# Optimization experiments

Hardware: AMD Instinct MI355X
Metric: run time of the kernel (lower is better)

## Reference

```python
import jax, jax.numpy as jnp
import numpy as np

DS = 32          # decoder_size
DIM = 512        # decoder_dim
NH = 8           # num_heads
HD = DIM // NH   # head_size = 64
NE = 4           # num_enc_reshape
NC = 2           # num_classes
B = 8
L = 2            # transformer layers
FF = 4 * DIM


def _ln(x, g, b):
    m = x.mean(-1, keepdims=True)
    v = x.var(-1, keepdims=True)
    return (x - m) / jnp.sqrt(v + 1e-5) * g + b


def _pos_bias(x_emb, y_emb, pad0, pad1):
    # 2D relative position encoding gathered from embeddings, shape [S2,S2,HD]
    ix = jnp.tile(jnp.arange(DS), DS)                       # column index per pixel
    iy = jnp.repeat(jnp.arange(DS), DS)                     # row index per pixel
    xd = jnp.clip(ix[None, :] - ix[:, None], -DS, DS) + DS  # [S2,S2] in [1,2*DS-1]
    yd = jnp.clip(iy[None, :] - iy[:, None], -DS, DS) + DS
    pos = x_emb[xd] + y_emb[yd]                              # [S2,S2,HD]
    S2 = DS * DS
    p0 = jnp.broadcast_to(pad0, (NE, NE, HD))
    p1 = jnp.broadcast_to(pad1, (S2, NE, HD))
    pos_pad = jnp.concatenate([p0, p1], axis=0)              # [S,NE,HD]
    right = jnp.concatenate([jnp.transpose(p1, (1, 0, 2)), pos], axis=0)  # [S,S2,HD]
    return jnp.concatenate([pos_pad, right], axis=1)         # [S,S,HD]


def _forward(x, patches, We, be, x_emb, y_emb, pad0, pad1,
             Wq, bq, Wk, bk, Wv, bv, Wo, bo,
             ln1_g, ln1_b, ln2_g, ln2_b, W1, b1, W2, b2, Wc, bc):
    b = x.shape[0]
    # patch embedding: [B,3,H,W] -> [B,H,W,3] -> Linear(3,DIM) -> [B,S2,DIM]
    p = jnp.transpose(patches, (0, 2, 3, 1))
    px = (p @ We + be).reshape(b, -1, DIM)
    xe = x.reshape(b, NE, DIM)
    h = jnp.concatenate([xe, px], axis=1)                    # [B,S,DIM]
    pos = _pos_bias(x_emb, y_emb, pad0, pad1)                # [S,S,HD]
    scale = 1.0 / jnp.sqrt(jnp.float32(HD))
    for l in range(L):
        hn = _ln(h, ln1_g[l], ln1_b[l])
        q = (hn @ Wq[l] + bq[l]).reshape(b, -1, NH, HD) * scale
        k = (hn @ Wk[l] + bk[l]).reshape(b, -1, NH, HD)
        v = (hn @ Wv[l] + bv[l]).reshape(b, -1, NH, HD)
        # content scores + gathered relative-position structure bias
        scores = jnp.einsum('bihd,bjhd->bhij', q, k) + jnp.einsum('bihd,ijd->bhij', q, pos)
        attn = jax.nn.softmax(scores, axis=-1)
        o = jnp.einsum('bhij,bjhd->bihd', attn, v).reshape(b, -1, DIM)
        h = h + (o @ Wo[l] + bo[l])
        hn = _ln(h, ln2_g[l], ln2_b[l])
        h = h + (jax.nn.relu(hn @ W1[l] + b1[l]) @ W2[l] + b2[l])
    out = h[:, NE:, :] @ Wc + bc                             # [B,S2,NC]
    out = out.reshape(b, DS, DS, NC)
    return jnp.transpose(out, (0, 3, 1, 2))                  # [B,NC,DS,DS]


def setup_inputs() -> dict:
    key = jax.random.key(0)
    ks = jax.random.split(key, 24)
    s = 0.02
    d = {}
    d['x'] = jax.random.normal(ks[0], (B, NE * DIM), jnp.float32)
    d['patches'] = jax.random.normal(ks[1], (B, 3, DS, DS), jnp.float32)
    d['We'] = jax.random.normal(ks[2], (3, DIM), jnp.float32) * s
    d['be'] = jnp.zeros((DIM,), jnp.float32)
    d['x_emb'] = jax.random.normal(ks[3], (2 * DS, HD), jnp.float32) * s
    d['y_emb'] = jax.random.normal(ks[4], (2 * DS, HD), jnp.float32) * s
    d['pad0'] = jax.random.normal(ks[5], (1, 1, HD), jnp.float32) * s
    d['pad1'] = jax.random.normal(ks[6], (1, 1, HD), jnp.float32) * s
    d['Wq'] = jax.random.normal(ks[7], (L, DIM, DIM), jnp.float32) * s
    d['bq'] = jnp.zeros((L, DIM), jnp.float32)
    d['Wk'] = jax.random.normal(ks[8], (L, DIM, DIM), jnp.float32) * s
    d['bk'] = jnp.zeros((L, DIM), jnp.float32)
    d['Wv'] = jax.random.normal(ks[9], (L, DIM, DIM), jnp.float32) * s
    d['bv'] = jnp.zeros((L, DIM), jnp.float32)
    d['Wo'] = jax.random.normal(ks[10], (L, DIM, DIM), jnp.float32) * s
    d['bo'] = jnp.zeros((L, DIM), jnp.float32)
    d['ln1_g'] = jnp.ones((L, DIM), jnp.float32)
    d['ln1_b'] = jnp.zeros((L, DIM), jnp.float32)
    d['ln2_g'] = jnp.ones((L, DIM), jnp.float32)
    d['ln2_b'] = jnp.zeros((L, DIM), jnp.float32)
    d['W1'] = jax.random.normal(ks[11], (L, DIM, FF), jnp.float32) * s
    d['b1'] = jnp.zeros((L, FF), jnp.float32)
    d['W2'] = jax.random.normal(ks[12], (L, FF, DIM), jnp.float32) * s
    d['b2'] = jnp.zeros((L, DIM), jnp.float32)
    d['Wc'] = jax.random.normal(ks[13], (DIM, NC), jnp.float32) * s
    d['bc'] = jnp.zeros((NC,), jnp.float32)
    return d


def reference(x, patches, We, be, x_emb, y_emb, pad0, pad1,
              Wq, bq, Wk, bk, Wv, bv, Wo, bo,
              ln1_g, ln1_b, ln2_g, ln2_b, W1, b1, W2, b2, Wc, bc):
    return _forward(x, patches, We, be, x_emb, y_emb, pad0, pad1,
                    Wq, bq, Wk, bk, Wv, bv, Wo, bo,
                    ln1_g, ln1_b, ln2_g, ln2_b, W1, b1, W2, b2, Wc, bc)
```

## Files before the change

kernel.cpp:

```cpp
#include <hip/hip_runtime.h>
#include <hip/hip_bf16.h>

#define DS 32
#define DIM 512
#define NH 8
#define HD 64
#define NE 4
#define NC 2
#define BB 8
#define LL 2
#define FFD 2048
#define S2 1024
#define SS 1028
#define MM (BB*SS)
#define KE 160
#define EXT ((size_t)BB*NH*SS*KE)

typedef __attribute__((ext_vector_type(8))) short s16x8;
typedef __attribute__((ext_vector_type(4))) float f32x4;
typedef unsigned short u16;

__device__ __forceinline__ u16 f2b(float f) {
    __hip_bfloat16 h = __float2bfloat16(f);
    return *reinterpret_cast<u16*>(&h);
}
__device__ __forceinline__ float b2f(u16 u) {
    __hip_bfloat16 h;
    *reinterpret_cast<u16*>(&h) = u;
    return __bfloat162float(h);
}

__global__ void embed_kernel(const float* __restrict__ x, const float* __restrict__ patches,
                             const float* __restrict__ We, const float* __restrict__ be,
                             float* __restrict__ h) {
    int row = blockIdx.x;
    int b = row / SS, i = row % SS;
    float* hr = h + (size_t)row * DIM;
    if (i < NE) {
        const float* xr = x + (size_t)b*NE*DIM + (size_t)i*DIM;
        for (int d = threadIdx.x; d < DIM; d += blockDim.x) hr[d] = xr[d];
    } else {
        int p = i - NE;
        float c0 = patches[(size_t)b*3*S2 + 0*S2 + p];
        float c1 = patches[(size_t)b*3*S2 + 1*S2 + p];
        float c2 = patches[(size_t)b*3*S2 + 2*S2 + p];
        for (int d = threadIdx.x; d < DIM; d += blockDim.x)
            hr[d] = be[d] + c0*We[d] + c1*We[DIM+d] + c2*We[2*DIM+d];
    }
}

__global__ void ln_kernel(const float* __restrict__ in, u16* __restrict__ out,
                          const float* __restrict__ g, const float* __restrict__ bt) {
    int row = blockIdx.x;
    const float* xr = in + (size_t)row*DIM;
    int t = threadIdx.x;
    float v0 = xr[t], v1 = xr[t+256];
    float s = v0 + v1, s2 = v0*v0 + v1*v1;
    for (int off = 32; off; off >>= 1) { s += __shfl_down(s, off); s2 += __shfl_down(s2, off); }
    __shared__ float ps[4], ps2[4];
    int wid = t >> 6, lane = t & 63;
    if (lane == 0) { ps[wid] = s; ps2[wid] = s2; }
    __syncthreads();
    if (t == 0) { ps[0] = ps[0]+ps[1]+ps[2]+ps[3]; ps2[0] = ps2[0]+ps2[1]+ps2[2]+ps2[3]; }
    __syncthreads();
    float mean = ps[0] * (1.0f/DIM);
    float var  = ps2[0] * (1.0f/DIM) - mean*mean;
    float inv = rsqrtf(var + 1e-5f);
    u16* orow = out + (size_t)row*DIM;
    orow[t]     = f2b((v0 - mean)*inv*g[t]     + bt[t]);
    orow[t+256] = f2b((v1 - mean)*inv*g[t+256] + bt[t+256]);
}

__global__ void transp_kernel(const float* __restrict__ src, u16* __restrict__ dst,
                              int R, int C) {
    __shared__ float tile[32][33];
    int c0 = blockIdx.x*32, r0 = blockIdx.y*32;
    int tx = threadIdx.x & 31, ty = threadIdx.x >> 5;
    #pragma unroll
    for (int ii = 0; ii < 4; ii++)
        tile[ty + ii*8][tx] = src[(size_t)(r0 + ty + ii*8)*C + c0 + tx];
    __syncthreads();
    #pragma unroll
    for (int ii = 0; ii < 4; ii++)
        dst[(size_t)(c0 + ty + ii*8)*R + r0 + tx] = f2b(tile[tx][ty + ii*8]);
}

__global__ void cat_bias_kernel(const float* __restrict__ bq, const float* __restrict__ bk,
                                const float* __restrict__ bv, float* __restrict__ out) {
    int t = blockIdx.x*256 + threadIdx.x;
    if (t >= 1536) return;
    out[t] = (t < 512) ? bq[t] : (t < 1024 ? bk[t-512] : bv[t-1024]);
}

template<int MODE, int RELU>
__global__ __launch_bounds__(256) void mfma_gemm(
    const u16* __restrict__ A, const u16* __restrict__ WT,
    const float* __restrict__ bias, const float* __restrict__ res,
    float* __restrict__ Cf, u16* __restrict__ Cb,
    u16* __restrict__ kd, u16* __restrict__ vd,
    int M, int N, int K)
{
    __shared__ __align__(16) u16 a_lds[128*64];
    __shared__ __align__(16) u16 b_lds[128*64];
    int row0 = blockIdx.x*128, col0 = blockIdx.y*128;
    int tid = threadIdx.x, w = tid>>6, l = tid&63;
    int lg = l>>4, lc = l&15;
    int wr = (w>>1)*64, wc = (w&1)*64;
    f32x4 acc[4][4];
    #pragma unroll
    for (int m = 0; m < 4; m++)
        #pragma unroll
        for (int n = 0; n < 4; n++) { f32x4 z = {0.f,0.f,0.f,0.f}; acc[m][n] = z; }

    s16x8 ar[4], br[4];
    #pragma unroll
    for (int p = 0; p < 4; p++) {
        int e = p*256 + tid;
        int r = e >> 3, c16 = e & 7;
        int ra = row0 + r; if (ra > M-1) ra = M-1;
        ar[p] = *(const s16x8*)(A  + (size_t)ra*K + c16*8);
        br[p] = *(const s16x8*)(WT + (size_t)(col0 + r)*K + c16*8);
    }

    for (int k0 = 0; k0 < K; k0 += 64) {
        #pragma unroll
        for (int p = 0; p < 4; p++) {
            int e = p*256 + tid;
            int r = e >> 3, c16 = e & 7;
            int ldso = r*128 + ((c16*16) ^ ((r&7)<<4));
            *(s16x8*)((char*)a_lds + ldso) = ar[p];
            *(s16x8*)((char*)b_lds + ldso) = br[p];
        }
        __syncthreads();
        int kn = k0 + 64;
        if (kn < K) {
            #pragma unroll
            for (int p = 0; p < 4; p++) {
                int e = p*256 + tid;
                int r = e >> 3, c16 = e & 7;
                int ra = row0 + r; if (ra > M-1) ra = M-1;
                ar[p] = *(const s16x8*)(A  + (size_t)ra*K + kn + c16*8);
                br[p] = *(const s16x8*)(WT + (size_t)(col0 + r)*K + kn + c16*8);
            }
        }
        #pragma unroll
        for (int ks = 0; ks < 2; ks++) {
            int cb = (ks*64 + lg*16) ^ ((l&7)<<4);
            s16x8 af[4], bfr[4];
            #pragma unroll
            for (int m = 0; m < 4; m++)
                af[m] = *(const s16x8*)((const char*)a_lds + (wr + m*16 + lc)*128 + cb);
            #pragma unroll
            for (int n = 0; n < 4; n++)
                bfr[n] = *(const s16x8*)((const char*)b_lds + (wc + n*16 + lc)*128 + cb);
            #pragma unroll
            for (int m = 0; m < 4; m++)
                #pragma unroll
                for (int n = 0; n < 4; n++)
                    acc[m][n] = __builtin_amdgcn_mfma_f32_16x16x32_bf16(af[m], bfr[n], acc[m][n], 0, 0, 0);
        }
        __syncthreads();
    }
    #pragma unroll
    for (int m = 0; m < 4; m++) {
        #pragma unroll
        for (int r = 0; r < 4; r++) {
            int row = row0 + wr + m*16 + lg*4 + r;
            if (row >= M) continue;
            #pragma unroll
            for (int n = 0; n < 4; n++) {
                int col = col0 + wc + n*16 + lc;
                float v = acc[m][n][r] + bias[col];
                if (MODE == 2) {
                    int which = col >> 9, c2 = col & 511;
                    if (which == 0) v *= 0.125f;
                    u16* dst = (which == 0) ? Cb : (which == 1 ? kd : vd);
                    dst[(size_t)row*512 + c2] = f2b(v);
                } else if (MODE == 1) {
                    if (RELU) v = fmaxf(v, 0.f);
                    Cb[(size_t)row*N + col] = f2b(v);
                } else {
                    Cf[(size_t)row*N + col] = v + res[(size_t)row*N + col];
                }
            }
        }
    }
}

__global__ void qp_kernel(const u16* __restrict__ q, const float* __restrict__ pad0,
                          const float* __restrict__ pad1, float* __restrict__ qp0,
                          float* __restrict__ qp1) {
    int idx = blockIdx.x * blockDim.x + threadIdx.x;
    if (idx >= BB*NH*SS) return;
    int i = idx % SS; int bh = idx / SS; int b = bh >> 3, hh = bh & 7;
    const u16* qr = q + ((size_t)(b*SS + i))*DIM + hh*HD;
    float a0 = 0.f, a1 = 0.f;
    #pragma unroll 8
    for (int d = 0; d < HD; d++) { float qv = b2f(qr[d]); a0 += qv*pad0[d]; a1 += qv*pad1[d]; }
    qp0[idx] = a0; qp1[idx] = a1;
}

__global__ void qext_kernel(const u16* __restrict__ qb, const float* __restrict__ qp0,
                            const float* __restrict__ qp1, u16* __restrict__ Qe) {
    size_t id = (size_t)blockIdx.x*256 + threadIdx.x;
    if (id >= EXT/8) return;
    int u = (int)(id % 20);
    size_t row = id / 20;
    int bh = (int)(row / SS), i = (int)(row - (size_t)bh*SS);
    int b = bh >> 3, hh = bh & 7;
    s16x8 val = {0,0,0,0,0,0,0,0};
    if (u < 8) {
        val = *(const s16x8*)(qb + ((size_t)(b*SS + i))*DIM + hh*HD + u*8);
    } else if (u == 16) {
        float v128 = (i < NE) ? qp0[bh*SS + i] : qp1[bh*SS + i];
        float v129 = (i < NE) ? qp1[bh*SS + i] : 0.f;
        val[0] = (short)f2b(v128);
        val[1] = (short)f2b(v129);
    }
    *(s16x8*)(Qe + row*KE + u*8) = val;
}

__global__ void kext_kernel(const u16* __restrict__ kb, u16* __restrict__ Ke) {
    size_t id = (size_t)blockIdx.x*256 + threadIdx.x;
    if (id >= EXT/8) return;
    int u = (int)(id % 20);
    size_t row = id / 20;
    int bh = (int)(row / SS), j = (int)(row - (size_t)bh*SS);
    int b = bh >> 3, hh = bh & 7;
    const short ONE = 0x3F80;
    s16x8 val = {0,0,0,0,0,0,0,0};
    if (u < 8) {
        val = *(const s16x8*)(kb + ((size_t)(b*SS + j))*DIM + hh*HD + u*8);
    } else {
        int pj = j - NE, cj = pj & 31, rj = pj >> 5;
        #pragma unroll
        for (int e = 0; e < 8; e++) {
            int t = u*8 + e;
            short v = 0;
            if (j >= NE) {
                if (t < 96)       { if (cj == t-64) v = ONE; }
                else if (t < 128) { if (rj == t-96) v = ONE; }
                else if (t == 129) v = ONE;
            } else if (t == 128) v = ONE;
            val[e] = v;
        }
    }
    *(s16x8*)(Ke + row*KE + u*8) = val;
}

__global__ __launch_bounds__(256) void qxy_mfma(
    const u16* __restrict__ q, const float* __restrict__ x_emb,
    const float* __restrict__ y_emb, u16* __restrict__ Qe)
{
    int tile = blockIdx.x, bh = blockIdx.y;
    int b = bh >> 3, hh = bh & 7;
    int tid = threadIdx.x, w = tid>>6, l = tid&63;
    int lg = l>>4, lc = l&15;
    int wr = (w>>1)*64, wc = (w&1)*64;
    int pi0 = tile*128;

    f32x4 acc[4][4];
    #pragma unroll
    for (int m = 0; m < 4; m++)
        #pragma unroll
        for (int n = 0; n < 4; n++) { f32x4 z = {0.f,0.f,0.f,0.f}; acc[m][n] = z; }

    s16x8 af[4][2];
    #pragma unroll
    for (int m = 0; m < 4; m++) {
        int pi = pi0 + wr + m*16 + lc;
        const u16* qp = q + ((size_t)(b*SS + NE + pi))*DIM + hh*HD + lg*8;
        af[m][0] = *(const s16x8*)qp;
        af[m][1] = *(const s16x8*)(qp + 32);
    }
    s16x8 bf[4][2];
    #pragma unroll
    for (int n = 0; n < 4; n++) {
        int tau = wc + n*16 + lc;
        const float* ep = (tau < 64) ? (x_emb + (size_t)tau*HD) : (y_emb + (size_t)(tau-64)*HD);
        #pragma unroll
        for (int ks = 0; ks < 2; ks++) {
            const float* e8 = ep + ks*32 + lg*8;
            s16x8 bv;
            #pragma unroll
            for (int t2 = 0; t2 < 8; t2++) bv[t2] = (short)f2b(e8[t2]);
            bf[n][ks] = bv;
        }
    }
    #pragma unroll
    for (int ks = 0; ks < 2; ks++)
        #pragma unroll
        for (int m = 0; m < 4; m++)
            #pragma unroll
            for (int n = 0; n < 4; n++)
                acc[m][n] = __builtin_amdgcn_mfma_f32_16x16x32_bf16(af[m][ks], bf[n][ks], acc[m][n], 0, 0, 0);

    #pragma unroll
    for (int m = 0; m < 4; m++) {
        #pragma unroll
        for (int r = 0; r < 4; r++) {
            int pi = pi0 + wr + m*16 + lg*4 + r;
            int ci = pi & 31, ri = pi >> 5;
            size_t rowbase = ((size_t)bh*SS + NE + pi)*KE;
            #pragma unroll
            for (int n = 0; n < 4; n++) {
                int tau = wc + n*16 + lc;
                float v = acc[m][n][r];
                if (tau < 64) {
                    int c = tau + ci - 32;
                    if (c >= 0 && c < 32) Qe[rowbase + 64 + c] = f2b(v);
                } else {
                    int c = (tau - 64) + ri - 32;
                    if (c >= 0 && c < 32) Qe[rowbase + 96 + c] = f2b(v);
                }
            }
        }
    }
}

#define KT 64
#define NKT 17
#define NQT 17
__global__ __launch_bounds__(256) void attn_mfma(
    const u16* __restrict__ Qe, const u16* __restrict__ Ke,
    const u16* __restrict__ v, u16* __restrict__ o)
{
    __shared__ __align__(16) u16 Kl[64*192];
    __shared__ __align__(16) u16 Vt[64][72];
    __shared__ __align__(16) u16 Pl[4][16][72];
    int qt = blockIdx.x, bh = blockIdx.y;
    int b = bh >> 3, hh = bh & 7;
    int tid = threadIdx.x, w = tid>>6, l = tid&63;
    int lg = l>>4, lc = l&15;
    int i0w = qt*64 + w*16;
    const s16x8 zs = {0,0,0,0,0,0,0,0};

    s16x8 qa[5];
    {
        int qrow = i0w + lc; if (qrow > SS-1) qrow = SS-1;
        const u16* qp = Qe + ((size_t)bh*SS + qrow)*KE + lg*8;
        #pragma unroll
        for (int ks = 0; ks < 5; ks++) qa[ks] = *(const s16x8*)(qp + ks*32);
    }

    float m_[4] = {-1e30f, -1e30f, -1e30f, -1e30f};
    float l_[4] = {0.f, 0.f, 0.f, 0.f};
    f32x4 oacc[4];
    #pragma unroll
    for (int f = 0; f < 4; f++) { f32x4 z = {0.f,0.f,0.f,0.f}; oacc[f] = z; }

    int skey = tid & 63, sd0 = (tid >> 6) * 16;

    for (int kt2 = 0; kt2 < NKT; kt2++) {
        int j0 = kt2 * KT;
        #pragma unroll
        for (int p = 0; p < 5; p++) {
            int e = p*256 + tid;
            int row = e / 20, u = e - row*20;
            int j = j0 + row;
            s16x8 kv = zs;
            if (j < SS) kv = *(const s16x8*)(Ke + ((size_t)bh*SS + j)*KE + u*8);
            *(s16x8*)((char*)Kl + row*384 + ((u ^ (row&7)) << 4)) = kv;
        }
        {
            int key = j0 + skey;
            uint4 v0 = {0,0,0,0}, v1 = {0,0,0,0};
            if (key < SS) {
                const uint4* vp = (const uint4*)(v + ((size_t)(b*SS + key))*DIM + hh*HD + sd0);
                v0 = vp[0]; v1 = vp[1];
            }
            const u16* pv = (const u16*)&v0;
            #pragma unroll
            for (int jj = 0; jj < 8; jj++) Vt[sd0 + jj][skey] = pv[jj];
            pv = (const u16*)&v1;
            #pragma unroll
            for (int jj = 0; jj < 8; jj++) Vt[sd0 + 8 + jj][skey] = pv[jj];
        }
        __syncthreads();

        f32x4 s[4];
        #pragma unroll
        for (int f = 0; f < 4; f++) { f32x4 z = {0.f,0.f,0.f,0.f}; s[f] = z; }
        #pragma unroll
        for (int ks = 0; ks < 5; ks++)
            #pragma unroll
            for (int f = 0; f < 4; f++) {
                int row = f*16 + lc;
                s16x8 kb2 = *(const s16x8*)((const char*)Kl + row*384 + ((((ks<<2)+lg) ^ (row&7)) << 4));
                s[f] = __builtin_amdgcn_mfma_f32_16x16x32_bf16(qa[ks], kb2, s[f], 0, 0, 0);
            }

        #pragma unroll
        for (int r = 0; r < 4; r++) {
            #pragma unroll
            for (int f = 0; f < 4; f++) {
                int j = j0 + f*16 + lc;
                if (j >= SS) s[f][r] = -1e30f;
            }
            float t4 = fmaxf(fmaxf(s[0][r], s[1][r]), fmaxf(s[2][r], s[3][r]));
            t4 = fmaxf(t4, __shfl_xor(t4, 1));
            t4 = fmaxf(t4, __shfl_xor(t4, 2));
            t4 = fmaxf(t4, __shfl_xor(t4, 4));
            t4 = fmaxf(t4, __shfl_xor(t4, 8));
            float mn = fmaxf(m_[r], t4);
            float sc = __expf(m_[r] - mn);
            m_[r] = mn;
            float rs = 0.f;
            #pragma unroll
            for (int f = 0; f < 4; f++) {
                float p = __expf(s[f][r] - mn);
                s[f][r] = p;
                rs += p;
            }
            rs += __shfl_xor(rs, 1); rs += __shfl_xor(rs, 2);
            rs += __shfl_xor(rs, 4); rs += __shfl_xor(rs, 8);
            l_[r] = l_[r]*sc + rs;
            #pragma unroll
            for (int f = 0; f < 4; f++) oacc[f][r] *= sc;
        }
        #pragma unroll
        for (int r = 0; r < 4; r++)
            #pragma unroll
            for (int f = 0; f < 4; f++)
                Pl[w][lg*4 + r][f*16 + lc] = f2b(s[f][r]);
        #pragma unroll
        for (int ks = 0; ks < 2; ks++) {
            s16x8 pa = *(const s16x8*)&Pl[w][lc][ks*32 + lg*8];
            #pragma unroll
            for (int f = 0; f < 4; f++) {
                s16x8 vb = *(const s16x8*)&Vt[f*16 + lc][ks*32 + lg*8];
                oacc[f] = __builtin_amdgcn_mfma_f32_16x16x32_bf16(pa, vb, oacc[f], 0, 0, 0);
            }
        }
        __syncthreads();
    }
    #pragma unroll
    for (int r = 0; r < 4; r++) {
        int i = i0w + lg*4 + r;
        if (i >= SS) continue;
        float inv = 1.0f / l_[r];
        #pragma unroll
        for (int f = 0; f < 4; f++)
            o[((size_t)(b*SS + i))*DIM + hh*HD + f*16 + lc] = f2b(oacc[f][r] * inv);
    }
}

__global__ void cls_kernel(const float* __restrict__ h, const float* __restrict__ Wc,
                           const float* __restrict__ bc, float* __restrict__ out) {
    int g = blockIdx.x*4 + (threadIdx.x >> 6);
    int lane = threadIdx.x & 63;
    if (g >= BB*S2) return;
    int b = g >> 10, p = g & 1023;
    const float* hr = h + ((size_t)(b*SS + NE + p))*DIM;
    float a0 = 0.f, a1 = 0.f;
    for (int d = lane; d < DIM; d += 64) {
        float hv = hr[d];
        a0 += hv * Wc[d*NC + 0];
        a1 += hv * Wc[d*NC + 1];
    }
    for (int off = 32; off; off >>= 1) { a0 += __shfl_down(a0, off); a1 += __shfl_down(a1, off); }
    if (lane == 0) {
        out[((size_t)(b*NC + 0))*S2 + p] = a0 + bc[0];
        out[((size_t)(b*NC + 1))*S2 + p] = a1 + bc[1];
    }
}

extern "C" void kernel_launch(void* const* d_in, const int* in_sizes, int n_in,
                              void* d_out, int out_size, void* d_ws, size_t ws_size,
                              hipStream_t stream) {
    const float* x      = (const float*)d_in[0];
    const float* patches= (const float*)d_in[1];
    const float* We     = (const float*)d_in[2];
    const float* be     = (const float*)d_in[3];
    const float* x_emb  = (const float*)d_in[4];
    const float* y_emb  = (const float*)d_in[5];
    const float* pad0   = (const float*)d_in[6];
    const float* pad1   = (const float*)d_in[7];
    const float* Wq     = (const float*)d_in[8];
    const float* bq     = (const float*)d_in[9];
    const float* Wk     = (const float*)d_in[10];
    const float* bk     = (const float*)d_in[11];
    const float* Wv     = (const float*)d_in[12];
    const float* bv     = (const float*)d_in[13];
    const float* Wo     = (const float*)d_in[14];
    const float* bo     = (const float*)d_in[15];
    const float* ln1_g  = (const float*)d_in[16];
    const float* ln1_b  = (const float*)d_in[17];
    const float* ln2_g  = (const float*)d_in[18];
    const float* ln2_b  = (const float*)d_in[19];
    const float* W1     = (const float*)d_in[20];
    const float* b1     = (const float*)d_in[21];
    const float* W2     = (const float*)d_in[22];
    const float* b2     = (const float*)d_in[23];
    const float* Wc     = (const float*)d_in[24];
    const float* bc     = (const float*)d_in[25];
    float* out = (float*)d_out;

    float* ws = (float*)d_ws;
    const size_t MD = (size_t)MM*DIM;
    float* h  = ws;
    u16* hn   = (u16*)(ws + MD);
    u16* qb   = (u16*)(ws + MD + MD/2);
    u16* kb   = qb + MD;
    u16* vb   = qb + 2*MD;
    u16* ob   = qb + 3*MD;
    u16* tb   = qb;
    u16* Qe   = (u16*)(ws + 3*MD + MD/2);
    u16* Ke   = Qe + EXT;
    float* after = ws + 3*MD + MD/2 + EXT;
    float* qp0 = after;
    float* qp1 = qp0 + 65792;
    float* bqkv = qp1 + 65792;
    u16* wt   = (u16*)(bqkv + 1536);

    const size_t WL = 3145728;

    for (int l = 0; l < LL; l++) {
        u16* base = wt + (size_t)l*WL;
        transp_kernel<<<dim3(16,16), 256, 0, stream>>>(Wq + (size_t)l*DIM*DIM, base + 0,        DIM, DIM);
        transp_kernel<<<dim3(16,16), 256, 0, stream>>>(Wk + (size_t)l*DIM*DIM, base + 262144,   DIM, DIM);
        transp_kernel<<<dim3(16,16), 256, 0, stream>>>(Wv + (size_t)l*DIM*DIM, base + 524288,   DIM, DIM);
        transp_kernel<<<dim3(16,16), 256, 0, stream>>>(Wo + (size_t)l*DIM*DIM, base + 786432,   DIM, DIM);
        transp_kernel<<<dim3(64,16), 256, 0, stream>>>(W1 + (size_t)l*DIM*FFD, base + 1048576,  DIM, FFD);
        transp_kernel<<<dim3(16,64), 256, 0, stream>>>(W2 + (size_t)l*FFD*DIM, base + 2097152,  FFD, DIM);
    }

    embed_kernel<<<MM, 256, 0, stream>>>(x, patches, We, be, h);

    dim3 gQKV(65, 12);
    dim3 g512(65, 4);
    dim3 gFF (65, 16);
    const int extUnits = (int)(EXT / 8);
    const int extBlocks = (extUnits + 255) / 256;

    for (int l = 0; l < LL; l++) {
        u16* base = wt + (size_t)l*WL;
        cat_bias_kernel<<<6, 256, 0, stream>>>(bq + (size_t)l*DIM, bk + (size_t)l*DIM, bv + (size_t)l*DIM, bqkv);
        ln_kernel<<<MM, 256, 0, stream>>>(h, hn, ln1_g + l*DIM, ln1_b + l*DIM);
        mfma_gemm<2,0><<<gQKV, 256, 0, stream>>>(hn, base, bqkv, nullptr, nullptr, qb, kb, vb, MM, 1536, DIM);
        qp_kernel<<<(BB*NH*SS + 255)/256, 256, 0, stream>>>(qb, pad0, pad1, qp0, qp1);
        qext_kernel<<<extBlocks, 256, 0, stream>>>(qb, qp0, qp1, Qe);
        qxy_mfma<<<dim3(8, BB*NH), 256, 0, stream>>>(qb, x_emb, y_emb, Qe);
        kext_kernel<<<extBlocks, 256, 0, stream>>>(kb, Ke);
        attn_mfma<<<dim3(NQT, BB*NH), 256, 0, stream>>>(Qe, Ke, vb, ob);
        mfma_gemm<0,0><<<g512, 256, 0, stream>>>(ob, base + 786432, bo + (size_t)l*DIM, h, h, nullptr, nullptr, nullptr, MM, DIM, DIM);
        ln_kernel<<<MM, 256, 0, stream>>>(h, hn, ln2_g + l*DIM, ln2_b + l*DIM);
        mfma_gemm<1,1><<<gFF, 256, 0, stream>>>(hn, base + 1048576, b1 + (size_t)l*FFD, nullptr, nullptr, tb, nullptr, nullptr, MM, FFD, DIM);
        mfma_gemm<0,0><<<g512, 256, 0, stream>>>(tb, base + 2097152, b2 + (size_t)l*DIM, h, h, nullptr, nullptr, nullptr, MM, DIM, FFD);
    }

    cls_kernel<<<(BB*S2)/4, 256, 0, stream>>>(h, Wc, bc, out);
}
```

Before: 724.6 us.

## Use direct global-to-LDS loads in GEMM, XCD-aware block remap, wider attention key tiles

The GEMM now loads A/B tiles straight into LDS with global_load_lds, dropping the register staging, the software prefetch and the XOR swizzle. It also switches to a 1D grid remapped so that consecutive tiles land on the same XCD, for better L2 locality. The attention kernel processes 128 keys per iteration instead of 64, halving the loop trips and barriers, and gets a similar XCD-grouped block mapping. The risks are more LDS bank conflicts from the unswizzled layout, lost global/compute overlap in the GEMM, and higher LDS and register use in attention.

Measured after the change: 860.2 us. +18.7%, slower.

```diff
diff --git a/kernel.cpp b/kernel.cpp
--- a/kernel.cpp
+++ b/kernel.cpp
@@ -28,6 +28,13 @@
     __hip_bfloat16 h;
     *reinterpret_cast<u16*>(&h) = u;
     return __bfloat162float(h);
+}
+
+__device__ __forceinline__ void gload_lds16(const void* g, void* l) {
+    __builtin_amdgcn_global_load_lds(
+        (const __attribute__((address_space(1))) void*)(uintptr_t)g,
+        (__attribute__((address_space(3))) void*)(uint32_t)(uintptr_t)l,
+        16, 0, 0);
 }
 
 __global__ void embed_kernel(const float* __restrict__ x, const float* __restrict__ patches,
@@ -98,11 +105,17 @@
     const float* __restrict__ bias, const float* __restrict__ res,
     float* __restrict__ Cf, u16* __restrict__ Cb,
     u16* __restrict__ kd, u16* __restrict__ vd,
-    int M, int N, int K)
+    int M, int N, int K, int Nt)
 {
     __shared__ __align__(16) u16 a_lds[128*64];
     __shared__ __align__(16) u16 b_lds[128*64];
-    int row0 = blockIdx.x*128, col0 = blockIdx.y*128;
+    int nwg = gridDim.x;
+    int q8 = nwg >> 3, r8 = nwg & 7;
+    int bid = blockIdx.x;
+    int xcd = bid & 7, loc = bid >> 3;
+    int g = (xcd < r8 ? xcd*(q8+1) : r8*(q8+1) + (xcd - r8)*q8) + loc;
+    int row0 = (g / Nt) * 128, col0 = (g % Nt) * 128;
+
     int tid = threadIdx.x, w = tid>>6, l = tid&63;
     int lg = l>>4, lc = l&15;
     int wr = (w>>1)*64, wc = (w&1)*64;
@@ -112,47 +125,27 @@
         #pragma unroll
         for (int n = 0; n < 4; n++) { f32x4 z = {0.f,0.f,0.f,0.f}; acc[m][n] = z; }
 
-    s16x8 ar[4], br[4];
-    #pragma unroll
-    for (int p = 0; p < 4; p++) {
-        int e = p*256 + tid;
-        int r = e >> 3, c16 = e & 7;
-        int ra = row0 + r; if (ra > M-1) ra = M-1;
-        ar[p] = *(const s16x8*)(A  + (size_t)ra*K + c16*8);
-        br[p] = *(const s16x8*)(WT + (size_t)(col0 + r)*K + c16*8);
-    }
-
+    int c16 = l & 7;
     for (int k0 = 0; k0 < K; k0 += 64) {
         #pragma unroll
         for (int p = 0; p < 4; p++) {
             int e = p*256 + tid;
-            int r = e >> 3, c16 = e & 7;
-            int ldso = r*128 + ((c16*16) ^ ((r&7)<<4));
-            *(s16x8*)((char*)a_lds + ldso) = ar[p];
-            *(s16x8*)((char*)b_lds + ldso) = br[p];
+            int r = e >> 3;
+            int ra = row0 + r; if (ra > M-1) ra = M-1;
+            gload_lds16(A  + (size_t)ra*K + k0 + c16*8,          a_lds + p*2048 + w*512);
+            gload_lds16(WT + (size_t)(col0 + r)*K + k0 + c16*8,  b_lds + p*2048 + w*512);
         }
         __syncthreads();
-        int kn = k0 + 64;
-        if (kn < K) {
-            #pragma unroll
-            for (int p = 0; p < 4; p++) {
-                int e = p*256 + tid;
-                int r = e >> 3, c16 = e & 7;
-                int ra = row0 + r; if (ra > M-1) ra = M-1;
-                ar[p] = *(const s16x8*)(A  + (size_t)ra*K + kn + c16*8);
-                br[p] = *(const s16x8*)(WT + (size_t)(col0 + r)*K + kn + c16*8);
-            }
-        }
         #pragma unroll
         for (int ks = 0; ks < 2; ks++) {
-            int cb = (ks*64 + lg*16) ^ ((l&7)<<4);
+            int cb = ks*32 + lg*8;
             s16x8 af[4], bfr[4];
             #pragma unroll
             for (int m = 0; m < 4; m++)
-                af[m] = *(const s16x8*)((const char*)a_lds + (wr + m*16 + lc)*128 + cb);
+                af[m] = *(const s16x8*)(a_lds + (wr + m*16 + lc)*64 + cb);
             #pragma unroll
             for (int n = 0; n < 4; n++)
-                bfr[n] = *(const s16x8*)((const char*)b_lds + (wc + n*16 + lc)*128 + cb);
+                bfr[n] = *(const s16x8*)(b_lds + (wc + n*16 + lc)*64 + cb);
             #pragma unroll
             for (int m = 0; m < 4; m++)
                 #pragma unroll
@@ -318,17 +311,19 @@
     }
 }
 
-#define KT 64
-#define NKT 17
+#define KT2 128
+#define NKT2 9
 #define NQT 17
 __global__ __launch_bounds__(256) void attn_mfma(
     const u16* __restrict__ Qe, const u16* __restrict__ Ke,
     const u16* __restrict__ v, u16* __restrict__ o)
 {
-    __shared__ __align__(16) u16 Kl[64*192];
-    __shared__ __align__(16) u16 Vt[64][72];
+    __shared__ __align__(16) u16 Kl[128*192];
+    __shared__ __align__(16) u16 Vt[2][64][72];
     __shared__ __align__(16) u16 Pl[4][16][72];
-    int qt = blockIdx.x, bh = blockIdx.y;
+    int bid = blockIdx.x;
+    int g = (bid & 7)*136 + (bid >> 3);
+    int qt = g % NQT, bh = g / NQT;
     int b = bh >> 3, hh = bh & 7;
     int tid = threadIdx.x, w = tid>>6, l = tid&63;
     int lg = l>>4, lc = l&15;
@@ -351,10 +346,10 @@
 
     int skey = tid & 63, sd0 = (tid >> 6) * 16;
 
-    for (int kt2 = 0; kt2 < NKT; kt2++) {
-        int j0 = kt2 * KT;
-        #pragma unroll
-        for (int p = 0; p < 5; p++) {
+    for (int kt2 = 0; kt2 < NKT2; kt2++) {
+        int j0 = kt2 * KT2;
+        #pragma unroll
+        for (int p = 0; p < 10; p++) {
             int e = p*256 + tid;
             int row = e / 20, u = e - row*20;
             int j = j0 + row;
@@ -362,8 +357,9 @@
             if (j < SS) kv = *(const s16x8*)(Ke + ((size_t)bh*SS + j)*KE + u*8);
             *(s16x8*)((char*)Kl + row*384 + ((u ^ (row&7)) << 4)) = kv;
         }
-        {
-            int key = j0 + skey;
+        #pragma unroll
+        for (int hb = 0; hb < 2; hb++) {
+            int key = j0 + hb*64 + skey;
             uint4 v0 = {0,0,0,0}, v1 = {0,0,0,0};
             if (key < SS) {
                 const uint4* vp = (const uint4*)(v + ((size_t)(b*SS + key))*DIM + hh*HD + sd0);
@@ -371,20 +367,20 @@
             }
             const u16* pv = (const u16*)&v0;
             #pragma unroll
-            for (int jj = 0; jj < 8; jj++) Vt[sd0 + jj][skey] = pv[jj];
+            for (int jj = 0; jj < 8; jj++) Vt[hb][sd0 + jj][skey] = pv[jj];
             pv = (const u16*)&v1;
             #pragma unroll
-            for (int jj = 0; jj < 8; jj++) Vt[sd0 + 8 + jj][skey] = pv[jj];
+            for (int jj = 0; jj < 8; jj++) Vt[hb][sd0 + 8 + jj][skey] = pv[jj];
         }
         __syncthreads();
 
-        f32x4 s[4];
-        #pragma unroll
-        for (int f = 0; f < 4; f++) { f32x4 z = {0.f,0.f,0.f,0.f}; s[f] = z; }
+        f32x4 s[8];
+        #pragma unroll
+        for (int f = 0; f < 8; f++) { f32x4 z = {0.f,0.f,0.f,0.f}; s[f] = z; }
         #pragma unroll
         for (int ks = 0; ks < 5; ks++)
             #pragma unroll
-            for (int f = 0; f < 4; f++) {
+            for (int f = 0; f < 8; f++) {
                 int row = f*16 + lc;
                 s16x8 kb2 = *(const s16x8*)((const char*)Kl + row*384 + ((((ks<<2)+lg) ^ (row&7)) << 4));
                 s[f] = __builtin_amdgcn_mfma_f32_16x16x32_bf16(qa[ks], kb2, s[f], 0, 0, 0);
@@ -393,11 +389,12 @@
         #pragma unroll
         for (int r = 0; r < 4; r++) {
             #pragma unroll
-            for (int f = 0; f < 4; f++) {
+            for (int f = 0; f < 8; f++) {
                 int j = j0 + f*16 + lc;
                 if (j >= SS) s[f][r] = -1e30f;
             }
-            float t4 = fmaxf(fmaxf(s[0][r], s[1][r]), fmaxf(s[2][r], s[3][r]));
+            float t4 = fmaxf(fmaxf(fmaxf(s[0][r], s[1][r]), fmaxf(s[2][r], s[3][r])),
+                             fmaxf(fmaxf(s[4][r], s[5][r]), fmaxf(s[6][r], s[7][r])));
             t4 = fmaxf(t4, __shfl_xor(t4, 1));
             t4 = fmaxf(t4, __shfl_xor(t4, 2));
             t4 = fmaxf(t4, __shfl_xor(t4, 4));
@@ -407,7 +404,7 @@
             m_[r] = mn;
             float rs = 0.f;
             #pragma unroll
-            for (int f = 0; f < 4; f++) {
+            for (int f = 0; f < 8; f++) {
                 float p = __expf(s[f][r] - mn);
                 s[f][r] = p;
                 rs += p;
@@ -419,17 +416,20 @@
             for (int f = 0; f < 4; f++) oacc[f][r] *= sc;
         }
         #pragma unroll
-        for (int r = 0; r < 4; r++)
-            #pragma unroll
-            for (int f = 0; f < 4; f++)
-                Pl[w][lg*4 + r][f*16 + lc] = f2b(s[f][r]);
-        #pragma unroll
-        for (int ks = 0; ks < 2; ks++) {
-            s16x8 pa = *(const s16x8*)&Pl[w][lc][ks*32 + lg*8];
-            #pragma unroll
-            for (int f = 0; f < 4; f++) {
-                s16x8 vb = *(const s16x8*)&Vt[f*16 + lc][ks*32 + lg*8];
-                oacc[f] = __builtin_amdgcn_mfma_f32_16x16x32_bf16(pa, vb, oacc[f], 0, 0, 0);
+        for (int hb = 0; hb < 2; hb++) {
+            #pragma unroll
+            for (int r = 0; r < 4; r++)
+                #pragma unroll
+                for (int f = 0; f < 4; f++)
+                    Pl[w][lg*4 + r][f*16 + lc] = f2b(s[hb*4 + f][r]);
+            #pragma unroll
+            for (int ks = 0; ks < 2; ks++) {
+                s16x8 pa = *(const s16x8*)&Pl[w][lc][ks*32 + lg*8];
+                #pragma unroll
+                for (int f = 0; f < 4; f++) {
+                    s16x8 vb = *(const s16x8*)&Vt[hb][f*16 + lc][ks*32 + lg*8];
+                    oacc[f] = __builtin_amdgcn_mfma_f32_16x16x32_bf16(pa, vb, oacc[f], 0, 0, 0);
+                }
             }
         }
         __syncthreads();
@@ -527,9 +527,6 @@
 
     embed_kernel<<<MM, 256, 0, stream>>>(x, patches, We, be, h);
 
-    dim3 gQKV(65, 12);
-    dim3 g512(65, 4);
-    dim3 gFF (65, 16);
     const int extUnits = (int)(EXT / 8);
     const int extBlocks = (extUnits + 255) / 256;
 
@@ -537,16 +534,16 @@
         u16* base = wt + (size_t)l*WL;
         cat_bias_kernel<<<6, 256, 0, stream>>>(bq + (size_t)l*DIM, bk + (size_t)l*DIM, bv + (size_t)l*DIM, bqkv);
         ln_kernel<<<MM, 256, 0, stream>>>(h, hn, ln1_g + l*DIM, ln1_b + l*DIM);
-        mfma_gemm<2,0><<<gQKV, 256, 0, stream>>>(hn, base, bqkv, nullptr, nullptr, qb, kb, vb, MM, 1536, DIM);
+        mfma_gemm<2,0><<<65*12, 256, 0, stream>>>(hn, base, bqkv, nullptr, nullptr, qb, kb, vb, MM, 1536, DIM, 12);
         qp_kernel<<<(BB*NH*SS + 255)/256, 256, 0, stream>>>(qb, pad0, pad1, qp0, qp1);
         qext_kernel<<<extBlocks, 256, 0, stream>>>(qb, qp0, qp1, Qe);
         qxy_mfma<<<dim3(8, BB*NH), 256, 0, stream>>>(qb, x_emb, y_emb, Qe);
         kext_kernel<<<extBlocks, 256, 0, stream>>>(kb, Ke);
-        attn_mfma<<<dim3(NQT, BB*NH), 256, 0, stream>>>(Qe, Ke, vb, ob);
-        mfma_gemm<0,0><<<g512, 256, 0, stream>>>(ob, base + 786432, bo + (size_t)l*DIM, h, h, nullptr, nullptr, nullptr, MM, DIM, DIM);
+        attn_mfma<<<NQT*BB*NH, 256, 0, stream>>>(Qe, Ke, vb, ob);
+        mfma_gemm<0,0><<<65*4, 256, 0, stream>>>(ob, base + 786432, bo + (size_t)l*DIM, h, h, nullptr, nullptr, nullptr, MM, DIM, DIM, 4);
         ln_kernel<<<MM, 256, 0, stream>>>(h, hn, ln2_g + l*DIM, ln2_b + l*DIM);
-        mfma_gemm<1,1><<<gFF, 256, 0, stream>>>(hn, base + 1048576, b1 + (size_t)l*FFD, nullptr, nullptr, tb, nullptr, nullptr, MM, FFD, DIM);
-        mfma_gemm<0,0><<<g512, 256, 0, stream>>>(tb, base + 2097152, b2 + (size_t)l*DIM, h, h, nullptr, nullptr, nullptr, MM, DIM, FFD);
+        mfma_gemm<1,1><<<65*16, 256, 0, stream>>>(hn, base + 1048576, b1 + (size_t)l*FFD, nullptr, nullptr, tb, nullptr, nullptr, MM, FFD, DIM, 16);
+        mfma_gemm<0,0><<<65*4, 256, 0, stream>>>(tb, base + 2097152, b2 + (size_t)l*DIM, h, h, nullptr, nullptr, nullptr, MM, DIM, FFD, 4);
     }
 
     cls_kernel<<<(BB*S2)/4, 256, 0, stream>>>(h, Wc, bc, out);
```
